# Optimization experiments

Measured on AMD Instinct MI355X. Metric: run time of the kernel, lower is better.

## Reference

```python
import jax, jax.numpy as jnp
import numpy as np

B, C, H, W = 4, 256, 96, 96
PARA, MOD, NH = 256, 256, 128
PI = 3.14159  # constant used in the torch source (not math.pi)


def setup_inputs():
    key = jax.random.key(0)
    ks = jax.random.split(key, 16)
    w = lambda k, shp: jax.random.normal(k, shp, jnp.float32) * 0.02
    z = lambda n: jnp.zeros((n,), jnp.float32)
    return {
        "feature_map": jax.random.normal(ks[0], (B, C, H, W), jnp.float32),
        "para_code": jax.random.normal(ks[1], (B, PARA), jnp.float32),
        "style_code": jax.random.normal(ks[2], (B, MOD), jnp.float32),
        "lin_common_w": w(ks[3], (PARA, PARA)), "lin_common_b": z(PARA),
        "lin_scale_w": w(ks[4], (PARA, C)), "lin_scale_b": z(C),
        "lin_rot_w": w(ks[5], (PARA, C)), "lin_rot_b": z(C),
        "lin_trans_w": w(ks[6], (PARA, 2 * C)), "lin_trans_b": z(2 * C),
        "a1_shared_w": w(ks[7], (MOD, NH)), "a1_shared_b": z(NH),
        "a1_gamma_w": w(ks[8], (NH, C)), "a1_gamma_b": z(C),
        "a1_beta_w": w(ks[9], (NH, C)), "a1_beta_b": z(C),
        "conv1_w": w(ks[10], (C, C, 3, 3)), "conv1_b": z(C),
        "a2_shared_w": w(ks[11], (MOD, NH)), "a2_shared_b": z(NH),
        "a2_gamma_w": w(ks[12], (NH, C)), "a2_gamma_b": z(C),
        "a2_beta_w": w(ks[13], (NH, C)), "a2_beta_b": z(C),
        "conv2_w": w(ks[14], (C, C, 3, 3)), "conv2_b": z(C),
    }


def _adaat(fm, pc, cw, cb, sw, sb, rw, rb, tw, tb):
    # fm: [B,C,H,W]; per-channel 2D affine warp, channels act as depth of a 3D grid_sample.
    Bn, Cn, Hn, Wn = fm.shape
    pc = jax.nn.relu(pc @ cw + cb)
    scale = jax.nn.sigmoid(pc @ sw + sb) * 2.0            # [B,C]
    angle = jnp.tanh(pc @ rw + rb) * PI                   # [B,C]
    trans = jnp.tanh(pc @ tw + tb).reshape(Bn, Cn, 2)     # [B,C,2]
    cos = jnp.cos(angle)[:, :, None, None]
    sin = jnp.sin(angle)[:, :, None, None]
    sc = scale[:, :, None, None]
    tx = trans[:, :, 0][:, :, None, None]
    ty = trans[:, :, 1][:, :, None, None]
    # align_corners=True style normalized source grid (as in make_coordinate_grid_3d)
    gx = (2.0 * jnp.arange(Wn) / (Wn - 1) - 1.0)[None, :]  # [1,W]
    gy = (2.0 * jnp.arange(Hn) / (Hn - 1) - 1.0)[:, None]  # [H,1]
    # rotation [[cos,-sin],[sin,cos]] @ [x,y], then scale + translate -> [B,C,H,W]
    xw = (cos * gx - sin * gy) * sc + tx
    yw = (sin * gx + cos * gy) * sc + ty
    gz = 2.0 * jnp.arange(Cn) / (Cn - 1) - 1.0             # [C]
    # unnormalize with align_corners=False (torch grid_sample default)
    ix = ((xw + 1.0) * Wn - 1.0) * 0.5
    iy = ((yw + 1.0) * Hn - 1.0) * 0.5
    iz = (((gz + 1.0) * Cn - 1.0) * 0.5)[None, :, None, None]  # [1,C,1,1]
    x0 = jnp.floor(ix); y0 = jnp.floor(iy); z0 = jnp.floor(iz)
    wx = ix - x0; wy = iy - y0; wz = iz - z0
    x0 = x0.astype(jnp.int32); y0 = y0.astype(jnp.int32); z0 = z0.astype(jnp.int32)
    bidx = jnp.arange(Bn)[:, None, None, None]

    def gather(zi, yi, xi):
        valid = (zi >= 0) & (zi < Cn) & (yi >= 0) & (yi < Hn) & (xi >= 0) & (xi < Wn)
        v = fm[bidx, jnp.clip(zi, 0, Cn - 1), jnp.clip(yi, 0, Hn - 1), jnp.clip(xi, 0, Wn - 1)]
        return jnp.where(valid, v, 0.0)

    out = jnp.zeros_like(fm)
    for dz, wzc in ((0, 1.0 - wz), (1, wz)):
        for dy, wyc in ((0, 1.0 - wy), (1, wy)):
            for dx, wxc in ((0, 1.0 - wx), (1, wx)):
                out = out + gather(z0 + dz, y0 + dy, x0 + dx) * (wzc * wyc * wxc)
    return out


def _adain_layer(x, style, shw, shb, gw, gb, bw, bb):
    m = x.mean(axis=(2, 3), keepdims=True)
    v = x.var(axis=(2, 3), keepdims=True)  # biased, as torch InstanceNorm2d
    xn = (x - m) / jnp.sqrt(v + 1e-5)
    a = jax.nn.relu(style @ shw + shb)
    gamma = (a @ gw + gb)[:, :, None, None]
    beta = (a @ bw + bb)[:, :, None, None]
    return xn * (1.0 + gamma) + beta


def _conv3(x, w, b):
    y = jax.lax.conv_general_dilated(x, w, (1, 1), ((1, 1), (1, 1)),
                                     dimension_numbers=("NCHW", "OIHW", "NCHW"))
    return y + b[None, :, None, None]


def _lrelu(x):
    return jnp.where(x >= 0, x, 0.2 * x)


def reference(feature_map, para_code, style_code,
              lin_common_w, lin_common_b, lin_scale_w, lin_scale_b,
              lin_rot_w, lin_rot_b, lin_trans_w, lin_trans_b,
              a1_shared_w, a1_shared_b, a1_gamma_w, a1_gamma_b, a1_beta_w, a1_beta_b,
              conv1_w, conv1_b,
              a2_shared_w, a2_shared_b, a2_gamma_w, a2_gamma_b, a2_beta_w, a2_beta_b,
              conv2_w, conv2_b):
    t = _adaat(feature_map, para_code, lin_common_w, lin_common_b,
               lin_scale_w, lin_scale_b, lin_rot_w, lin_rot_b, lin_trans_w, lin_trans_b)
    x = _adain_layer(t, style_code, a1_shared_w, a1_shared_b, a1_gamma_w, a1_gamma_b, a1_beta_w, a1_beta_b)
    x = _conv3(_lrelu(x), conv1_w, conv1_b)
    x = _adain_layer(x, style_code, a2_shared_w, a2_shared_b, a2_gamma_w, a2_gamma_b, a2_beta_w, a2_beta_b)
    x = _conv3(_lrelu(x), conv2_w, conv2_b)
    return x
```

## Files before the change

### kernel.cpp

```cpp
#include <hip/hip_runtime.h>
#include <hip/hip_bf16.h>
#include <cstddef>

#define BATCH 4
#define CH 256
#define HH 96
#define WW 96
#define HWN (HH*WW)
#define NTOT (BATCH*CH*HWN)
#define XT_H 98
#define XT_W 98
#define XT_PLANE (XT_H*XT_W*CH)

typedef __attribute__((ext_vector_type(16))) float f32x16;
typedef __attribute__((ext_vector_type(8))) __bf16 bfrag;
typedef __attribute__((ext_vector_type(8))) unsigned short u16x8;

static __device__ __forceinline__ unsigned short f2bf(float f) {
  unsigned int u = __float_as_uint(f);
  unsigned int r = (u + 0x7fffu + ((u >> 16) & 1u)) >> 16;
  return (unsigned short)r;
}

__global__ __launch_bounds__(256) void params_stage1_kernel(
    const float* __restrict__ para, const float* __restrict__ style,
    const float* __restrict__ cw,  const float* __restrict__ cb,
    const float* __restrict__ a1w, const float* __restrict__ a1b,
    const float* __restrict__ a2w, const float* __restrict__ a2b,
    float* __restrict__ pcbuf, float* __restrict__ a1buf, float* __restrict__ a2buf)
{
  __shared__ float s_in[256];
  __shared__ float red[256];
  int part = blockIdx.x, b = blockIdx.y, t = threadIdx.x;
  s_in[t] = (part < 4) ? para[b*256 + t] : style[b*256 + t];
  __syncthreads();
  if (part < 4) {
    int o = t & 63, ks = t >> 6, co0 = part * 64;
    const float* wcol = cw + co0 + o;
    float acc = 0.f;
    #pragma unroll 8
    for (int i = 0; i < 64; i++) {
      int k = ks * 64 + i;
      acc = fmaf(s_in[k], wcol[k * 256], acc);
    }
    red[t] = acc;
    __syncthreads();
    if (t < 64) {
      float s = red[t] + red[t + 64] + red[t + 128] + red[t + 192];
      pcbuf[b*256 + co0 + t] = fmaxf(s + cb[co0 + t], 0.f);
    }
  } else {
    const float* w  = (part == 4) ? a1w : a2w;
    const float* bb = (part == 4) ? a1b : a2b;
    float* outp = (part == 4) ? a1buf : a2buf;
    int o = t & 127, ks = t >> 7;
    const float* wcol = w + o;
    float acc = 0.f;
    #pragma unroll 8
    for (int i = 0; i < 128; i++) {
      int k = ks * 128 + i;
      acc = fmaf(s_in[k], wcol[k * 128], acc);
    }
    red[t] = acc;
    __syncthreads();
    if (t < 128) {
      float s = red[t] + red[t + 128];
      outp[b*128 + t] = fmaxf(s + bb[t], 0.f);
    }
  }
}

__global__ __launch_bounds__(256) void params_stage2_kernel(
    const float* __restrict__ pcbuf, const float* __restrict__ a1buf,
    const float* __restrict__ a2buf,
    const float* __restrict__ sw,  const float* __restrict__ sb,
    const float* __restrict__ rw,  const float* __restrict__ rb,
    const float* __restrict__ tw,  const float* __restrict__ tb,
    const float* __restrict__ g1w, const float* __restrict__ g1b,
    const float* __restrict__ b1w, const float* __restrict__ b1b,
    const float* __restrict__ g2w, const float* __restrict__ g2b,
    const float* __restrict__ b2w, const float* __restrict__ b2b,
    float* __restrict__ warp, float* __restrict__ gb1, float* __restrict__ gb2)
{
  __shared__ float s_pc[256], s_a1[128], s_a2[128];
  __shared__ float red[8][4][16];
  int co0 = blockIdx.x * 16, b = blockIdx.y, t = threadIdx.x;
  s_pc[t] = pcbuf[b*256 + t];
  if (t < 128) s_a1[t] = a1buf[b*128 + t];
  else         s_a2[t - 128] = a2buf[b*128 + (t - 128)];
  __syncthreads();

  int cl = t & 15, klane = t >> 4;
  int c = co0 + cl;
  const float2* tw2 = (const float2*)tw;
  float ds = 0.f, dr = 0.f, dtx = 0.f, dty = 0.f;
  float g1 = 0.f, be1 = 0.f, g2 = 0.f, be2 = 0.f;
  #pragma unroll 4
  for (int kk = 0; kk < 16; kk++) {
    int i = klane * 16 + kk;
    float p = s_pc[i];
    ds  = fmaf(p, sw[i*256 + c], ds);
    dr  = fmaf(p, rw[i*256 + c], dr);
    float2 tv = tw2[i*256 + c];
    dtx = fmaf(p, tv.x, dtx);
    dty = fmaf(p, tv.y, dty);
  }
  #pragma unroll 4
  for (int kk = 0; kk < 8; kk++) {
    int i = klane * 8 + kk;
    float a = s_a1[i];
    g1  = fmaf(a, g1w[i*256 + c], g1);
    be1 = fmaf(a, b1w[i*256 + c], be1);
    float a2v = s_a2[i];
    g2  = fmaf(a2v, g2w[i*256 + c], g2);
    be2 = fmaf(a2v, b2w[i*256 + c], be2);
  }
  ds  += __shfl_down(ds, 32, 64);  ds  += __shfl_down(ds, 16, 64);
  dr  += __shfl_down(dr, 32, 64);  dr  += __shfl_down(dr, 16, 64);
  dtx += __shfl_down(dtx, 32, 64); dtx += __shfl_down(dtx, 16, 64);
  dty += __shfl_down(dty, 32, 64); dty += __shfl_down(dty, 16, 64);
  g1  += __shfl_down(g1, 32, 64);  g1  += __shfl_down(g1, 16, 64);
  be1 += __shfl_down(be1, 32, 64); be1 += __shfl_down(be1, 16, 64);
  g2  += __shfl_down(g2, 32, 64);  g2  += __shfl_down(g2, 16, 64);
  be2 += __shfl_down(be2, 32, 64); be2 += __shfl_down(be2, 16, 64);
  int wv = t >> 6;
  if ((t & 63) < 16) {
    red[0][wv][cl] = ds;  red[1][wv][cl] = dr;
    red[2][wv][cl] = dtx; red[3][wv][cl] = dty;
    red[4][wv][cl] = g1;  red[5][wv][cl] = be1;
    red[6][wv][cl] = g2;  red[7][wv][cl] = be2;
  }
  __syncthreads();
  if (t < 16) {
    float v[8];
    #pragma unroll
    for (int o = 0; o < 8; o++)
      v[o] = red[o][0][t] + red[o][1][t] + red[o][2][t] + red[o][3][t];
    int cc = co0 + t;
    int bc = b*256 + cc;
    float scale = 2.f / (1.f + expf(-(v[0] + sb[cc])));
    float ang = tanhf(v[1] + rb[cc]) * 3.14159f;
    float sn, cs;
    sincosf(ang, &sn, &cs);
    warp[bc*4 + 0] = cs * scale;
    warp[bc*4 + 1] = sn * scale;
    warp[bc*4 + 2] = tanhf(v[2] + tb[2*cc]);
    warp[bc*4 + 3] = tanhf(v[3] + tb[2*cc + 1]);
    gb1[bc*2]     = v[4] + g1b[cc];
    gb1[bc*2 + 1] = v[5] + b1b[cc];
    gb2[bc*2]     = v[6] + g2b[cc];
    gb2[bc*2 + 1] = v[7] + b2b[cc];
  }
}

__global__ __launch_bounds__(256) void prep_weights_kernel(
    const float* __restrict__ w1, const float* __restrict__ w2,
    unsigned short* __restrict__ wf1, unsigned short* __restrict__ wf2)
{
  int co = blockIdx.x & 255;
  const float* src = (blockIdx.x < 256) ? w1 : w2;
  unsigned short* dst = (blockIdx.x < 256) ? wf1 : wf2;
  int ci = threadIdx.x;
  int coblk = co >> 6, m = (co >> 5) & 1;
  int l = (co & 31) | (((ci >> 3) & 1) << 5);
  int ks = ci >> 4, j = ci & 7;
  const float* p = src + ((size_t)co * 256 + ci) * 9;
  #pragma unroll
  for (int tap = 0; tap < 9; tap++) {
    size_t idx = (((size_t)((coblk * 16 + ks) * 9 + tap) * 2 + m) * 64 + l) * 8 + j;
    dst[idx] = f2bf(p[tap]);
  }
}

__global__ __launch_bounds__(256) void adaat_kernel(
    const float* __restrict__ fm, const float* __restrict__ warp,
    const float* __restrict__ gb1, float* __restrict__ tout,
    float* __restrict__ nrm1)
{
  __shared__ float s[96 * 100];
  int bc = blockIdx.x;
  int b = bc >> 8, c = bc & 255;
  float csc = warp[bc*4 + 0], ssc = warp[bc*4 + 1];
  float tx = warp[bc*4 + 2], ty = warp[bc*4 + 3];

  const float axw = csc * (96.f / 95.f);
  const float axh = -ssc * (96.f / 95.f);
  const float ax0 = 48.f * (tx - csc + ssc) + 47.5f;
  const float ayw = ssc * (96.f / 95.f);
  const float ayh = csc * (96.f / 95.f);
  const float ay0 = 48.f * (ty - ssc - csc) + 47.5f;

  float iz = 256.f * (float)c / 255.f - 0.5f;
  float z0f = floorf(iz);
  float wz = iz - z0f;
  int z0 = (int)z0f;
  const float* p0 = (z0 >= 0) ? fm + (size_t)(b*256 + z0) * HWN : nullptr;
  const float* p1 = (z0 + 1 < 256) ? fm + (size_t)(b*256 + z0 + 1) * HWN : nullptr;
  float w0 = 1.f - wz, w1 = wz;

  int t = threadIdx.x;
  const float4* q0 = (const float4*)p0;
  const float4* q1 = (const float4*)p1;
  for (int i = t; i < 2304; i += 256) {
    int row = i / 24, col = i - row * 24;
    float4 r = {0.f, 0.f, 0.f, 0.f};
    if (q0) {
      float4 v = q0[i];
      r.x = w0 * v.x; r.y = w0 * v.y; r.z = w0 * v.z; r.w = w0 * v.w;
    }
    if (q1) {
      float4 v = q1[i];
      r.x = fmaf(w1, v.x, r.x); r.y = fmaf(w1, v.y, r.y);
      r.z = fmaf(w1, v.z, r.z); r.w = fmaf(w1, v.w, r.w);
    }
    *(float4*)&s[row * 100 + col * 4] = r;
  }
  __syncthreads();

  int h = t / 96, w = t - (t / 96) * 96;
  float* dst = tout + (size_t)bc * HWN;
  float sum = 0.f, sumsq = 0.f;
  #pragma unroll
  for (int k = 0; k < 36; k++) {
    float ix = fmaf(axw, (float)w, fmaf(axh, (float)h, ax0));
    float iy = fmaf(ayw, (float)w, fmaf(ayh, (float)h, ay0));
    float x0f = floorf(ix), y0f = floorf(iy);
    float wx = ix - x0f, wy = iy - y0f;
    int x0 = (int)x0f, y0 = (int)y0f;
    int x0c = min(max(x0, 0), 95), x1c = min(max(x0 + 1, 0), 95);
    int y0c = min(max(y0, 0), 95), y1c = min(max(y0 + 1, 0), 95);
    bool vx0 = (unsigned)x0 < 96u, vx1 = (unsigned)(x0 + 1) < 96u;
    bool vy0 = (unsigned)y0 < 96u, vy1 = (unsigned)(y0 + 1) < 96u;
    float a00 = s[y0c * 100 + x0c], a01 = s[y0c * 100 + x1c];
    float a10 = s[y1c * 100 + x0c], a11 = s[y1c * 100 + x1c];
    float wxm = 1.f - wx, wym = 1.f - wy;
    float w00 = (vy0 && vx0) ? wym * wxm : 0.f;
    float w01 = (vy0 && vx1) ? wym * wx  : 0.f;
    float w10 = (vy1 && vx0) ? wy * wxm  : 0.f;
    float w11 = (vy1 && vx1) ? wy * wx   : 0.f;
    float v = w00 * a00;
    v = fmaf(w01, a01, v);
    v = fmaf(w10, a10, v);
    v = fmaf(w11, a11, v);
    dst[t + k * 256] = v;
    sum += v;
    sumsq = fmaf(v, v, sumsq);
    int wn = w + 64;
    int carry = (wn >= 96) ? 1 : 0;
    w = wn - (carry ? 96 : 0);
    h += 2 + carry;
  }

  for (int off = 32; off > 0; off >>= 1) {
    sum   += __shfl_down(sum, off, 64);
    sumsq += __shfl_down(sumsq, off, 64);
  }
  __shared__ float rs[4], rq[4];
  int lane = t & 63, wvi = t >> 6;
  if (lane == 0) { rs[wvi] = sum; rq[wvi] = sumsq; }
  __syncthreads();
  if (t == 0) {
    float S = rs[0] + rs[1] + rs[2] + rs[3];
    float Q = rq[0] + rq[1] + rq[2] + rq[3];
    float m = S * (1.f / 9216.f);
    float var = Q * (1.f / 9216.f) - m * m;
    float rstd = rsqrtf(var + 1e-5f);
    float sc = (1.f + gb1[bc*2]) * rstd;
    nrm1[bc*2] = sc;
    nrm1[bc*2 + 1] = gb1[bc*2 + 1] - m * sc;
  }
}

__global__ __launch_bounds__(256) void stats_kernel(
    const float* __restrict__ x, const float* __restrict__ gb,
    float* __restrict__ nrm)
{
  int bc = blockIdx.x;
  const float4* p = (const float4*)(x + (size_t)bc * HWN);
  float sum = 0.f, sumsq = 0.f;
  for (int i = threadIdx.x; i < HWN / 4; i += 256) {
    float4 v = p[i];
    sum   += v.x + v.y + v.z + v.w;
    sumsq += v.x*v.x + v.y*v.y + v.z*v.z + v.w*v.w;
  }
  for (int off = 32; off > 0; off >>= 1) {
    sum   += __shfl_down(sum, off, 64);
    sumsq += __shfl_down(sumsq, off, 64);
  }
  __shared__ float rs[4], rq[4];
  int lane = threadIdx.x & 63, wv = threadIdx.x >> 6;
  if (lane == 0) { rs[wv] = sum; rq[wv] = sumsq; }
  __syncthreads();
  if (threadIdx.x == 0) {
    float S = rs[0] + rs[1] + rs[2] + rs[3];
    float Q = rq[0] + rq[1] + rq[2] + rq[3];
    float m = S * (1.f / 9216.f);
    float var = Q * (1.f / 9216.f) - m * m;
    float rstd = rsqrtf(var + 1e-5f);
    float sc = (1.f + gb[bc*2]) * rstd;
    nrm[bc*2] = sc;
    nrm[bc*2 + 1] = gb[bc*2 + 1] - m * sc;
  }
}

__global__ __launch_bounds__(256) void transpose_norm_kernel(
    const float* __restrict__ x, const float* __restrict__ nrm,
    unsigned short* __restrict__ xt)
{
  int hi = blockIdx.x;
  int b  = blockIdx.y;
  unsigned short* dst = xt + (size_t)b * XT_PLANE + (size_t)hi * (XT_W * CH);
  int t = threadIdx.x;
  int h = hi - 1;
  u16x8 zero = {0,0,0,0,0,0,0,0};
  if (h < 0 || h >= 96) {
    for (int c = t; c < XT_W * CH / 8; c += 256) ((u16x8*)dst)[c] = zero;
    return;
  }
  __shared__ unsigned short s[96 * 256];
  int ci = t;
  float sc = nrm[(b*256 + ci)*2], bi = nrm[(b*256 + ci)*2 + 1];
  const float* src = x + ((size_t)(b*256 + ci)) * HWN + h * 96;
  for (int wg = 0; wg < 24; wg++) {
    float4 v = *(const float4*)(src + wg * 4);
    float y0 = fmaf(v.x, sc, bi); y0 = (y0 >= 0.f) ? y0 : 0.2f * y0;
    float y1 = fmaf(v.y, sc, bi); y1 = (y1 >= 0.f) ? y1 : 0.2f * y1;
    float y2 = fmaf(v.z, sc, bi); y2 = (y2 >= 0.f) ? y2 : 0.2f * y2;
    float y3 = fmaf(v.w, sc, bi); y3 = (y3 >= 0.f) ? y3 : 0.2f * y3;
    s[(wg*4 + 0) * 256 + ci] = f2bf(y0);
    s[(wg*4 + 1) * 256 + ci] = f2bf(y1);
    s[(wg*4 + 2) * 256 + ci] = f2bf(y2);
    s[(wg*4 + 3) * 256 + ci] = f2bf(y3);
  }
  __syncthreads();
  for (int c = t; c < 98 * 32; c += 256) {
    int w = c >> 5, p = c & 31;
    u16x8 v = zero;
    if (w >= 1 && w <= 96) v = *(const u16x8*)&s[(w - 1) * 256 + p * 8];
    ((u16x8*)dst)[c] = v;
  }
}

__global__ __launch_bounds__(256, 3) void conv_mfma_kernel(
    const unsigned short* __restrict__ xt,
    const unsigned short* __restrict__ wf,
    const float* __restrict__ cb,
    float* __restrict__ out)
{
  __shared__ __align__(16) unsigned short s_in[2][784 * 8];

  int hb = blockIdx.x, coblk = blockIdx.y, b = blockIdx.z;
  int co0 = coblk * 64, h0 = hb * 2;
  int t = threadIdx.x, lane = t & 63, wv = t >> 6;
  int rw = wv >> 1, mh = wv & 1;
  int l31 = lane & 31, lhi = lane >> 5;
  const unsigned short* xtb = xt + (size_t)b * XT_PLANE;

  int pre_g[4];
  #pragma unroll
  for (int i = 0; i < 4; i++) {
    int c = t + i * 256;
    if (c < 784) {
      int r = c / 196;
      int rem = c - r * 196;
      int half = rem / 98;
      int w = rem - half * 98;
      pre_g[i] = ((h0 + r) * 98 + w) * 256 + half * 8;
    }
  }

  f32x16 acc[3];
  #pragma unroll
  for (int n = 0; n < 3; n++)
    #pragma unroll
    for (int i = 0; i < 16; i++) acc[n][i] = 0.f;

  const unsigned short* wfb = wf + (size_t)(coblk * 16) * 9216 + mh * 512 + lane * 8;

  u16x8 stg[4];
  #pragma unroll
  for (int i = 0; i < 3; i++) stg[i] = *(const u16x8*)(xtb + pre_g[i]);
  if (t < 16) stg[3] = *(const u16x8*)(xtb + pre_g[3]);
  #pragma unroll
  for (int i = 0; i < 3; i++) *(u16x8*)(&s_in[0][(t + i * 256) * 8]) = stg[i];
  if (t < 16) *(u16x8*)(&s_in[0][(t + 3 * 256) * 8]) = stg[3];

  bfrag wa[9];
  #pragma unroll
  for (int tap = 0; tap < 9; tap++) wa[tap] = *(const bfrag*)(wfb + tap * 1024);

  #pragma unroll
  for (int i = 0; i < 3; i++) stg[i] = *(const u16x8*)(xtb + pre_g[i] + 16);
  if (t < 16) stg[3] = *(const u16x8*)(xtb + pre_g[3] + 16);
  __syncthreads();

  int buf = 0;
  #pragma unroll 1
  for (int ks = 0; ks < 16; ks++) {
    const unsigned short* sb = s_in[buf];
    int ksn = (ks < 15) ? (ks + 1) : 15;
    const unsigned short* wkn = wfb + (size_t)ksn * 9216;
    #pragma unroll
    for (int ky = 0; ky < 3; ky++) {
      const unsigned short* srow = sb + (((rw + ky) * 2 + lhi) * 98) * 8;
      bfrag bb[9];
      #pragma unroll
      for (int kx = 0; kx < 3; kx++)
        #pragma unroll
        for (int n = 0; n < 3; n++)
          bb[kx * 3 + n] = *(const bfrag*)(srow + (n * 32 + kx + l31) * 8);
      #pragma unroll
      for (int kx = 0; kx < 3; kx++) {
        int tap = ky * 3 + kx;
        acc[0] = __builtin_amdgcn_mfma_f32_32x32x16_bf16(wa[tap], bb[kx*3+0], acc[0], 0, 0, 0);
        acc[1] = __builtin_amdgcn_mfma_f32_32x32x16_bf16(wa[tap], bb[kx*3+1], acc[1], 0, 0, 0);
        acc[2] = __builtin_amdgcn_mfma_f32_32x32x16_bf16(wa[tap], bb[kx*3+2], acc[2], 0, 0, 0);
        wa[tap] = *(const bfrag*)(wkn + tap * 1024);
      }
    }
    if (ks < 15) {
      unsigned short* sn = s_in[buf ^ 1];
      #pragma unroll
      for (int i = 0; i < 3; i++) *(u16x8*)(&sn[(t + i * 256) * 8]) = stg[i];
      if (t < 16) *(u16x8*)(&sn[(t + 3 * 256) * 8]) = stg[3];
      if (ks < 14) {
        int off = (ks + 2) * 16;
        #pragma unroll
        for (int i = 0; i < 3; i++) stg[i] = *(const u16x8*)(xtb + pre_g[i] + off);
        if (t < 16) stg[3] = *(const u16x8*)(xtb + pre_g[3] + off);
      }
    }
    __syncthreads();
    buf ^= 1;
  }

  int h = h0 + rw;
  #pragma unroll
  for (int r = 0; r < 16; r++) {
    int row = (r & 3) + 8 * (r >> 2) + 4 * lhi;
    int co = co0 + mh * 32 + row;
    float bv = cb[co];
    size_t base = ((size_t)(b * 256 + co) * 96 + h) * 96;
    #pragma unroll
    for (int n = 0; n < 3; n++) {
      out[base + n * 32 + l31] = acc[n][r] + bv;
    }
  }
}

extern "C" void kernel_launch(void* const* d_in, const int* in_sizes, int n_in,
                              void* d_out, int out_size, void* d_ws, size_t ws_size,
                              hipStream_t stream)
{
  const float* fm    = (const float*)d_in[0];
  const float* para  = (const float*)d_in[1];
  const float* style = (const float*)d_in[2];
  const float* cw  = (const float*)d_in[3];
  const float* cb  = (const float*)d_in[4];
  const float* sw  = (const float*)d_in[5];
  const float* sb  = (const float*)d_in[6];
  const float* rw  = (const float*)d_in[7];
  const float* rb  = (const float*)d_in[8];
  const float* tw  = (const float*)d_in[9];
  const float* tb  = (const float*)d_in[10];
  const float* a1w = (const float*)d_in[11];
  const float* a1b = (const float*)d_in[12];
  const float* g1w = (const float*)d_in[13];
  const float* g1b = (const float*)d_in[14];
  const float* b1w = (const float*)d_in[15];
  const float* b1b = (const float*)d_in[16];
  const float* c1w = (const float*)d_in[17];
  const float* c1b = (const float*)d_in[18];
  const float* a2w = (const float*)d_in[19];
  const float* a2b = (const float*)d_in[20];
  const float* g2w = (const float*)d_in[21];
  const float* g2b = (const float*)d_in[22];
  const float* b2w = (const float*)d_in[23];
  const float* b2b = (const float*)d_in[24];
  const float* c2w = (const float*)d_in[25];
  const float* c2b = (const float*)d_in[26];

  float* outf = (float*)d_out;

  unsigned short* xtbuf = (unsigned short*)d_ws;
  unsigned short* wf1   = xtbuf + (size_t)BATCH * XT_PLANE;
  unsigned short* wf2   = wf1 + 9 * 256 * 256;
  float* fws  = (float*)(wf2 + 9 * 256 * 256);
  float* warp = fws;
  float* gb1  = warp + 4 * 1024;
  float* gb2  = gb1 + 2 * 1024;
  float* nrm1 = gb2 + 2 * 1024;
  float* nrm2 = nrm1 + 2 * 1024;
  float* pcbuf = nrm2 + 2 * 1024;
  float* a1buf = pcbuf + 1024;
  float* a2buf = a1buf + 512;

  params_stage1_kernel<<<dim3(6, 4), 256, 0, stream>>>(para, style, cw, cb,
      a1w, a1b, a2w, a2b, pcbuf, a1buf, a2buf);
  params_stage2_kernel<<<dim3(16, 4), 256, 0, stream>>>(pcbuf, a1buf, a2buf,
      sw, sb, rw, rb, tw, tb, g1w, g1b, b1w, b1b, g2w, g2b, b2w, b2b,
      warp, gb1, gb2);
  prep_weights_kernel<<<512, 256, 0, stream>>>(c1w, c2w, wf1, wf2);
  adaat_kernel<<<1024, 256, 0, stream>>>(fm, warp, gb1, outf, nrm1);
  transpose_norm_kernel<<<dim3(98, 4), 256, 0, stream>>>(outf, nrm1, xtbuf);
  conv_mfma_kernel<<<dim3(48, 4, 4), 256, 0, stream>>>(xtbuf, wf1, c1b, outf);
  stats_kernel<<<1024, 256, 0, stream>>>(outf, gb2, nrm2);
  transpose_norm_kernel<<<dim3(98, 4), 256, 0, stream>>>(outf, nrm2, xtbuf);
  conv_mfma_kernel<<<dim3(48, 4, 4), 256, 0, stream>>>(xtbuf, wf2, c2b, outf);
}
```

Before: 191.3 us.

## Fuse AdaIN stats into conv epilogue and stage inputs via direct global-to-LDS loads

The conv epilogue now reduces per-channel sum and sum of squares across lanes and writes partials for each row, so a tiny finalize kernel replaces the full stats pass that reread the 38 MB conv1 output. The conv input staging switches from register-staged copies to global_load_lds direct-to-LDS loads issued at the top of each k-step. It also raises wave priority around the MFMA block. This removes one full memory pass and frees staging registers. The cost is extra shuffle work in the epilogue, and the single-pass variance formula on partial sums carries some precision risk.

```diff
diff --git a/kernel.cpp b/kernel.cpp
--- a/kernel.cpp
+++ b/kernel.cpp
@@ -20,6 +20,13 @@
   unsigned int u = __float_as_uint(f);
   unsigned int r = (u + 0x7fffu + ((u >> 16) & 1u)) >> 16;
   return (unsigned short)r;
+}
+
+static __device__ __forceinline__ void gload16(const unsigned short* g,
+                                               unsigned short* l) {
+  __builtin_amdgcn_global_load_lds(
+      (const __attribute__((address_space(1))) unsigned int*)g,
+      (__attribute__((address_space(3))) unsigned int*)l, 16, 0, 0);
 }
 
 __global__ __launch_bounds__(256) void params_stage1_kernel(
@@ -271,36 +278,24 @@
   }
 }
 
-__global__ __launch_bounds__(256) void stats_kernel(
-    const float* __restrict__ x, const float* __restrict__ gb,
+__global__ __launch_bounds__(256) void finalize_stats_kernel(
+    const float* __restrict__ psum, const float* __restrict__ gb,
     float* __restrict__ nrm)
 {
-  int bc = blockIdx.x;
-  const float4* p = (const float4*)(x + (size_t)bc * HWN);
-  float sum = 0.f, sumsq = 0.f;
-  for (int i = threadIdx.x; i < HWN / 4; i += 256) {
-    float4 v = p[i];
-    sum   += v.x + v.y + v.z + v.w;
-    sumsq += v.x*v.x + v.y*v.y + v.z*v.z + v.w*v.w;
-  }
-  for (int off = 32; off > 0; off >>= 1) {
-    sum   += __shfl_down(sum, off, 64);
-    sumsq += __shfl_down(sumsq, off, 64);
-  }
-  __shared__ float rs[4], rq[4];
-  int lane = threadIdx.x & 63, wv = threadIdx.x >> 6;
-  if (lane == 0) { rs[wv] = sum; rq[wv] = sumsq; }
-  __syncthreads();
-  if (threadIdx.x == 0) {
-    float S = rs[0] + rs[1] + rs[2] + rs[3];
-    float Q = rq[0] + rq[1] + rq[2] + rq[3];
-    float m = S * (1.f / 9216.f);
-    float var = Q * (1.f / 9216.f) - m * m;
-    float rstd = rsqrtf(var + 1e-5f);
-    float sc = (1.f + gb[bc*2]) * rstd;
-    nrm[bc*2] = sc;
-    nrm[bc*2 + 1] = gb[bc*2 + 1] - m * sc;
-  }
+  int bc = blockIdx.x * 256 + threadIdx.x;
+  int b = bc >> 8, co = bc & 255;
+  float S = 0.f, Q = 0.f;
+  for (int j = 0; j < 96; j++) {
+    const float* p = psum + ((((size_t)b * 48 + (j >> 1)) * 2 + (j & 1)) * 256 + co) * 2;
+    S += p[0];
+    Q += p[1];
+  }
+  float m = S * (1.f / 9216.f);
+  float var = Q * (1.f / 9216.f) - m * m;
+  float rstd = rsqrtf(var + 1e-5f);
+  float sc = (1.f + gb[bc*2]) * rstd;
+  nrm[bc*2] = sc;
+  nrm[bc*2 + 1] = gb[bc*2 + 1] - m * sc;
 }
 
 __global__ __launch_bounds__(256) void transpose_norm_kernel(
@@ -345,7 +340,8 @@
     const unsigned short* __restrict__ xt,
     const unsigned short* __restrict__ wf,
     const float* __restrict__ cb,
-    float* __restrict__ out)
+    float* __restrict__ out,
+    float* __restrict__ psum)
 {
   __shared__ __align__(16) unsigned short s_in[2][784 * 8];
 
@@ -377,26 +373,31 @@
 
   const unsigned short* wfb = wf + (size_t)(coblk * 16) * 9216 + mh * 512 + lane * 8;
 
-  u16x8 stg[4];
-  #pragma unroll
-  for (int i = 0; i < 3; i++) stg[i] = *(const u16x8*)(xtb + pre_g[i]);
-  if (t < 16) stg[3] = *(const u16x8*)(xtb + pre_g[3]);
-  #pragma unroll
-  for (int i = 0; i < 3; i++) *(u16x8*)(&s_in[0][(t + i * 256) * 8]) = stg[i];
-  if (t < 16) *(u16x8*)(&s_in[0][(t + 3 * 256) * 8]) = stg[3];
-
+  {
+    #pragma unroll
+    for (int i = 0; i < 3; i++)
+      gload16(xtb + pre_g[i], &s_in[0][(i * 256 + wv * 64) * 8]);
+    u16x8 tail;
+    if (t < 16) tail = *(const u16x8*)(xtb + pre_g[3]);
+    if (t < 16) *(u16x8*)(&s_in[0][(768 + t) * 8]) = tail;
+  }
   bfrag wa[9];
   #pragma unroll
   for (int tap = 0; tap < 9; tap++) wa[tap] = *(const bfrag*)(wfb + tap * 1024);
-
-  #pragma unroll
-  for (int i = 0; i < 3; i++) stg[i] = *(const u16x8*)(xtb + pre_g[i] + 16);
-  if (t < 16) stg[3] = *(const u16x8*)(xtb + pre_g[3] + 16);
   __syncthreads();
 
   int buf = 0;
+  u16x8 tail;
   #pragma unroll 1
   for (int ks = 0; ks < 16; ks++) {
+    if (ks < 15) {
+      int cib = (ks + 1) * 16;
+      unsigned short* nb = s_in[buf ^ 1];
+      #pragma unroll
+      for (int i = 0; i < 3; i++)
+        gload16(xtb + pre_g[i] + cib, &nb[(i * 256 + wv * 64) * 8]);
+      if (t < 16) tail = *(const u16x8*)(xtb + pre_g[3] + cib);
+    }
     const unsigned short* sb = s_in[buf];
     int ksn = (ks < 15) ? (ks + 1) : 15;
     const unsigned short* wkn = wfb + (size_t)ksn * 9216;
@@ -409,6 +410,7 @@
         #pragma unroll
         for (int n = 0; n < 3; n++)
           bb[kx * 3 + n] = *(const bfrag*)(srow + (n * 32 + kx + l31) * 8);
+      __builtin_amdgcn_s_setprio(1);
       #pragma unroll
       for (int kx = 0; kx < 3; kx++) {
         int tap = ky * 3 + kx;
@@ -417,33 +419,51 @@
         acc[2] = __builtin_amdgcn_mfma_f32_32x32x16_bf16(wa[tap], bb[kx*3+2], acc[2], 0, 0, 0);
         wa[tap] = *(const bfrag*)(wkn + tap * 1024);
       }
-    }
-    if (ks < 15) {
-      unsigned short* sn = s_in[buf ^ 1];
-      #pragma unroll
-      for (int i = 0; i < 3; i++) *(u16x8*)(&sn[(t + i * 256) * 8]) = stg[i];
-      if (t < 16) *(u16x8*)(&sn[(t + 3 * 256) * 8]) = stg[3];
-      if (ks < 14) {
-        int off = (ks + 2) * 16;
-        #pragma unroll
-        for (int i = 0; i < 3; i++) stg[i] = *(const u16x8*)(xtb + pre_g[i] + off);
-        if (t < 16) stg[3] = *(const u16x8*)(xtb + pre_g[3] + off);
-      }
-    }
+      __builtin_amdgcn_s_setprio(0);
+    }
+    if (ks < 15 && t < 16) *(u16x8*)(&s_in[buf ^ 1][(768 + t) * 8]) = tail;
     __syncthreads();
     buf ^= 1;
   }
 
   int h = h0 + rw;
+  float bsum[16], bsq[16];
   #pragma unroll
   for (int r = 0; r < 16; r++) {
     int row = (r & 3) + 8 * (r >> 2) + 4 * lhi;
     int co = co0 + mh * 32 + row;
     float bv = cb[co];
     size_t base = ((size_t)(b * 256 + co) * 96 + h) * 96;
+    float s = 0.f, q = 0.f;
     #pragma unroll
     for (int n = 0; n < 3; n++) {
-      out[base + n * 32 + l31] = acc[n][r] + bv;
+      float y = acc[n][r] + bv;
+      out[base + n * 32 + l31] = y;
+      s += y;
+      q = fmaf(y, y, q);
+    }
+    bsum[r] = s; bsq[r] = q;
+  }
+  if (psum) {
+    #pragma unroll
+    for (int r = 0; r < 16; r++) {
+      float s = bsum[r], q = bsq[r];
+      #pragma unroll
+      for (int off = 16; off > 0; off >>= 1) {
+        s += __shfl_xor(s, off, 64);
+        q += __shfl_xor(q, off, 64);
+      }
+      bsum[r] = s; bsq[r] = q;
+    }
+    if (l31 == 0) {
+      float* pp = psum + ((((size_t)b * 48 + hb) * 2 + rw) * 256) * 2;
+      #pragma unroll
+      for (int r = 0; r < 16; r++) {
+        int row = (r & 3) + 8 * (r >> 2) + 4 * lhi;
+        int co = co0 + mh * 32 + row;
+        pp[co * 2]     = bsum[r];
+        pp[co * 2 + 1] = bsq[r];
+      }
     }
   }
 }
@@ -494,6 +514,7 @@
   float* pcbuf = nrm2 + 2 * 1024;
   float* a1buf = pcbuf + 1024;
   float* a2buf = a1buf + 512;
+  float* psum  = a2buf + 512;
 
   params_stage1_kernel<<<dim3(6, 4), 256, 0, stream>>>(para, style, cw, cb,
       a1w, a1b, a2w, a2b, pcbuf, a1buf, a2buf);
@@ -503,8 +524,8 @@
   prep_weights_kernel<<<512, 256, 0, stream>>>(c1w, c2w, wf1, wf2);
   adaat_kernel<<<1024, 256, 0, stream>>>(fm, warp, gb1, outf, nrm1);
   transpose_norm_kernel<<<dim3(98, 4), 256, 0, stream>>>(outf, nrm1, xtbuf);
-  conv_mfma_kernel<<<dim3(48, 4, 4), 256, 0, stream>>>(xtbuf, wf1, c1b, outf);
-  stats_kernel<<<1024, 256, 0, stream>>>(outf, gb2, nrm2);
+  conv_mfma_kernel<<<dim3(48, 4, 4), 256, 0, stream>>>(xtbuf, wf1, c1b, outf, psum);
+  finalize_stats_kernel<<<4, 256, 0, stream>>>(psum, gb2, nrm2);
   transpose_norm_kernel<<<dim3(98, 4), 256, 0, stream>>>(outf, nrm2, xtbuf);
-  conv_mfma_kernel<<<dim3(48, 4, 4), 256, 0, stream>>>(xtbuf, wf2, c2b, outf);
-}
+  conv_mfma_kernel<<<dim3(48, 4, 4), 256, 0, stream>>>(xtbuf, wf2, c2b, outf, nullptr);
+}
```

New measurement: 188.9 us. Within noise of the previous version (-1.3%).
